# Optimization experiments

Hardware: AMD Instinct MI355X
Metric: run time of the kernel (lower is better)

## Reference

```python
import jax, jax.numpy as jnp
import numpy as np

B, T, E = 4096, 200, 64
H1, H2 = 80, 40


def setup_inputs() -> dict:
    key = jax.random.key(0)
    ks = jax.random.split(key, 9)
    query = jax.random.normal(ks[0], (B, 1, E), dtype=jnp.float32)
    keys = jax.random.normal(ks[1], (B, T, E), dtype=jnp.float32)
    keys_length = jax.random.randint(ks[2], (B,), 0, T, dtype=jnp.int64)
    # DNN params (init_std=1 in original, but any values work for a reference)
    W1 = jax.random.normal(ks[3], (4 * E, H1), dtype=jnp.float32) * 0.05
    b1 = jnp.zeros((H1,), dtype=jnp.float32)
    W2 = jax.random.normal(ks[4], (H1, H2), dtype=jnp.float32) * 0.05
    b2 = jnp.zeros((H2,), dtype=jnp.float32)
    Wd = jax.random.normal(ks[5], (H2, 1), dtype=jnp.float32) * 0.05
    bd = jnp.zeros((1,), dtype=jnp.float32)
    return {"query": query, "keys": keys, "keys_length": keys_length,
            "W1": W1, "b1": b1, "W2": W2, "b2": b2, "Wd": Wd, "bd": bd}


def reference(query, keys, keys_length, W1, b1, W2, b2, Wd, bd):
    # Local activation unit: expand query over T, build 4-way concat feature
    q = jnp.broadcast_to(query, keys.shape)                 # [B,T,E]
    att_in = jnp.concatenate([q, keys, q - keys, q * keys], axis=-1)  # [B,T,4E]
    # Small MLP with sigmoid activations (DNN), then linear head -> score
    h = jax.nn.sigmoid(jnp.einsum('btk,kh->bth', att_in, W1) + b1)
    h = jax.nn.sigmoid(jnp.einsum('btk,kh->bth', h, W2) + b2)
    score = jnp.einsum('btk,ko->bto', h, Wd) + bd           # [B,T,1]
    outputs = jnp.swapaxes(score, 1, 2)                     # [B,1,T]
    # length mask (supports_masking=False path)
    mask = (jnp.arange(keys.shape[1]) < keys_length[:, None])[:, None, :]  # [B,1,T]
    # weight_normalization=False -> masked positions get 0
    outputs = jnp.where(mask, outputs, jnp.zeros_like(outputs))
    # weighted sum pooling over history
    return jnp.matmul(outputs, keys)                        # [B,1,E]
```

## Files before the change

kernel.cpp:

```cpp
#include <hip/hip_runtime.h>

typedef float f32x4 __attribute__((ext_vector_type(4)));
typedef short bf16x8 __attribute__((ext_vector_type(8)));

#define T_LEN 200
#define E_DIM 64
#define H1D 80
#define H2D 40
#define T_PAD 208
#define NT1 5
#define NT2 3
#define WS_BC    0u
#define WS_D     20480u
#define WS_W2    40960u
#define WS_W1EFF 50176u
#define WS_BIAS  70656u

static __device__ __forceinline__ unsigned short f2bf(float x) {
  unsigned u = __builtin_bit_cast(unsigned, x);
  return (unsigned short)((u + 0x7fffu + ((u >> 16) & 1u)) >> 16);
}
static __device__ __forceinline__ float bf2f(unsigned short h) {
  unsigned u = ((unsigned)h) << 16;
  return __builtin_bit_cast(float, u);
}
static __device__ __forceinline__ float sigm(float x) {
  return __builtin_amdgcn_rcpf(1.f + __expf(-x));
}

__global__ __launch_bounds__(256)
void setup1(const float* __restrict__ W1, const float* __restrict__ W2,
            unsigned char* __restrict__ ws) {
  float* bc = (float*)(ws + WS_BC);
  float* dd = (float*)(ws + WS_D);
  unsigned short* w2f = (unsigned short*)(ws + WS_W2);
  float* w1e = (float*)(ws + WS_W1EFF);
  int g = blockIdx.x * 256 + threadIdx.x;
  if (g < 5120) {
    int nt = g >> 10;
    int rem = g & 1023;
    int ks = rem >> 9;
    int l = (rem >> 3) & 63;
    int j = g & 7;
    int e = ks * 32 + ((l >> 4) << 3) + j;
    int col = nt * 16 + (l & 15);
    bc[g] = W1[(64 + e) * H1D + col] - W1[(128 + e) * H1D + col];
    dd[g] = W1[(192 + e) * H1D + col];
  } else if (g < 9728) {
    int h = g - 5120;
    int nt2 = h / 1536;
    int rem = h - nt2 * 1536;
    int ks2 = rem >> 9;
    int l = (rem >> 3) & 63;
    int j = h & 7;
    int k = ks2 * 32 + ((l >> 4) << 3) + j;
    int n = nt2 * 16 + (l & 15);
    float v = (k < H1D && n < H2D) ? W2[k * H2D + n] : 0.f;
    w2f[h] = f2bf(v);
  } else if (g < 14848) {
    int w = g - 9728;
    int e = w / 80;
    int j = w - e * 80;
    w1e[w] = W1[e * H1D + j] + W1[(128 + e) * H1D + j];
  }
}

__global__ __launch_bounds__(128)
void setup2(const float* __restrict__ query, const float* __restrict__ b1,
            const unsigned char* __restrict__ ws, float* __restrict__ bias) {
  const float* w1e = (const float*)(ws + WS_W1EFF);
  const int b = blockIdx.x, j = threadIdx.x;
  if (j < H1D) {
    float s = b1[j];
    const float* q = query + (size_t)b * E_DIM;
    #pragma unroll
    for (int e = 0; e < E_DIM; ++e) s += q[e] * w1e[e * H1D + j];
    bias[(size_t)b * H1D + j] = s;
  }
}

#define OFF_K   0
#define OFF_H1  26624
#define OFF_FR  47104
#define OFF_SC  57344
#define OFF_PP  58176
#define OFF_QS  60224
#define OFF_B1  60480
#define SMEM_TOTAL 60800

template <bool BW>
__global__ __launch_bounds__(512, 2)
void din_main(const float* __restrict__ query, const float* __restrict__ keys,
              const int* __restrict__ keys_length,
              const float* __restrict__ b1, const float* __restrict__ b2,
              const float* __restrict__ Wd, const float* __restrict__ bd,
              const unsigned char* __restrict__ ws, float* __restrict__ out) {
  __shared__ __align__(16) unsigned char smem[SMEM_TOTAL];
  unsigned char* Kb  = smem + OFF_K;
  unsigned char* H1b = smem + OFF_H1;
  unsigned short* FR = (unsigned short*)(smem + OFF_FR);
  float* SC = (float*)(smem + OFF_SC);
  float* PP = (float*)(smem + OFF_PP);
  float* QS = (float*)(smem + OFF_QS);
  float* B1 = (float*)(smem + OFF_B1);

  const int tid = threadIdx.x, b = blockIdx.x;
  const int lane = tid & 63, wv = tid >> 6;
  const int qq = lane >> 4, cc = lane & 15;
  const float* keyb = keys + (size_t)b * (T_LEN * E_DIM);

  if (!BW && tid < E_DIM) QS[tid] = query[(size_t)b * E_DIM + tid];

  #pragma unroll
  for (int it = 0; it < 7; ++it) {
    int f = (it * 512 + tid) * 4;
    if (f < T_LEN * E_DIM) {
      const float4 v = *(const float4*)(keyb + f);
      unsigned p0 = ((unsigned)f2bf(v.y) << 16) | f2bf(v.x);
      unsigned p1 = ((unsigned)f2bf(v.w) << 16) | f2bf(v.z);
      int row = f >> 6;
      unsigned byte = ((unsigned)(f * 2)) ^ ((unsigned)(row & 7) << 4);
      *(uint2*)(Kb + byte) = make_uint2(p0, p1);
    } else if (f < T_PAD * E_DIM) {
      int row = f >> 6;
      unsigned byte = ((unsigned)(f * 2)) ^ ((unsigned)(row & 7) << 4);
      *(uint2*)(Kb + byte) = make_uint2(0u, 0u);
    }
  }

  {
    const float* wsBC = (const float*)(ws + WS_BC);
    const float* wsD  = (const float*)(ws + WS_D);
    const float* qrow = query + (size_t)b * E_DIM;
    #pragma unroll
    for (int i = 0; i < 10; ++i) {
      int f = i * 512 + tid;
      int j = f & 7, l = (f >> 3) & 63, ks = (f >> 9) & 1;
      int e = ks * 32 + ((l >> 4) << 3) + j;
      FR[f] = f2bf(wsBC[f] + qrow[e] * wsD[f]);
    }
  }

  float bia[NT1];
  if (BW) {
    const float* wbias = (const float*)(ws + WS_BIAS);
    #pragma unroll
    for (int nt = 0; nt < NT1; ++nt) bia[nt] = wbias[(size_t)b * H1D + nt * 16 + cc];
  }
  float b2c[NT2], wdl[NT2];
  #pragma unroll
  for (int nt = 0; nt < NT2; ++nt) {
    int col = nt * 16 + cc;
    b2c[nt] = (col < H2D) ? b2[col] : 0.f;
    wdl[nt] = (col < H2D) ? Wd[col] : 0.f;
  }
  const float bdv = bd[0];
  const int len = keys_length[b];

  __syncthreads();

  if (!BW) {
    if (tid < H1D) {
      const float* w1e = (const float*)(ws + WS_W1EFF);
      float s = b1[tid];
      #pragma unroll
      for (int e = 0; e < E_DIM; ++e) s += QS[e] * w1e[e * H1D + tid];
      B1[tid] = s;
    }
    __syncthreads();
    #pragma unroll
    for (int nt = 0; nt < NT1; ++nt) bia[nt] = B1[nt * 16 + cc];
  }

  const unsigned short* wsW2 = (const unsigned short*)(ws + WS_W2);
  unsigned char* H1w = H1b + wv * 2560;
  #pragma unroll
  for (int ti = 0; ti < 2; ++ti) {
    const int tt = wv + ti * 8;
    if (tt < 13) {
      const unsigned krow = (unsigned)(tt * 16 + cc);
      const unsigned ksw = (krow & 7u) << 4;
      bf16x8 a0 = *(const bf16x8*)(Kb + ((krow * 128 + qq * 16) ^ ksw));
      bf16x8 a1 = *(const bf16x8*)(Kb + ((krow * 128 + 64 + qq * 16) ^ ksw));
      f32x4 accs[NT1];
      #pragma unroll
      for (int nt = 0; nt < NT1; ++nt) {
        bf16x8 bf0 = *(const bf16x8*)(FR + ((nt * 2 + 0) * 64 + lane) * 8);
        bf16x8 bf1 = *(const bf16x8*)(FR + ((nt * 2 + 1) * 64 + lane) * 8);
        f32x4 a = {bia[nt], bia[nt], bia[nt], bia[nt]};
        a = __builtin_amdgcn_mfma_f32_16x16x32_bf16(a0, bf0, a, 0, 0, 0);
        a = __builtin_amdgcn_mfma_f32_16x16x32_bf16(a1, bf1, a, 0, 0, 0);
        accs[nt] = a;
      }
      #pragma unroll
      for (int nt = 0; nt < NT1; ++nt) {
        #pragma unroll
        for (int r = 0; r < 4; ++r) {
          int rloc = qq * 4 + r;
          unsigned byte = ((unsigned)(rloc * 160 + (nt * 16 + cc) * 2)) ^ ((unsigned)(rloc & 7) << 4);
          *(unsigned short*)(H1w + byte) = f2bf(sigm(accs[nt][r]));
        }
      }
      const unsigned hsw = ((unsigned)cc & 7u) << 4;
      const unsigned hb = (unsigned)cc * 160;
      bf16x8 h0 = *(const bf16x8*)(H1w + ((hb + qq * 16) ^ hsw));
      bf16x8 h1 = *(const bf16x8*)(H1w + ((hb + 64 + qq * 16) ^ hsw));
      bf16x8 h2 = {0, 0, 0, 0, 0, 0, 0, 0};
      if (qq < 2) h2 = *(const bf16x8*)(H1w + ((hb + 128 + qq * 16) ^ hsw));
      float vr[4] = {0.f, 0.f, 0.f, 0.f};
      #pragma unroll
      for (int nt = 0; nt < NT2; ++nt) {
        bf16x8 w0 = *(const bf16x8*)(wsW2 + ((nt * 3 + 0) * 64 + lane) * 8);
        bf16x8 w1 = *(const bf16x8*)(wsW2 + ((nt * 3 + 1) * 64 + lane) * 8);
        bf16x8 w2 = *(const bf16x8*)(wsW2 + ((nt * 3 + 2) * 64 + lane) * 8);
        f32x4 a = {b2c[nt], b2c[nt], b2c[nt], b2c[nt]};
        a = __builtin_amdgcn_mfma_f32_16x16x32_bf16(h0, w0, a, 0, 0, 0);
        a = __builtin_amdgcn_mfma_f32_16x16x32_bf16(h1, w1, a, 0, 0, 0);
        a = __builtin_amdgcn_mfma_f32_16x16x32_bf16(h2, w2, a, 0, 0, 0);
        #pragma unroll
        for (int r = 0; r < 4; ++r) vr[r] += sigm(a[r]) * wdl[nt];
      }
      #pragma unroll
      for (int r = 0; r < 4; ++r) {
        float v = vr[r];
        v += __shfl_xor(v, 1);
        v += __shfl_xor(v, 2);
        v += __shfl_xor(v, 4);
        v += __shfl_xor(v, 8);
        if (cc == 0) {
          int t = tt * 16 + qq * 4 + r;
          SC[t] = (t < len) ? (bdv + v) : 0.f;
        }
      }
    }
  }
  __syncthreads();

  {
    const int e = tid & 63;
    const int t0 = tid >> 6;
    float accp = 0.f;
    #pragma unroll
    for (int i = 0; i < 25; ++i) {
      int t = t0 + i * 8;
      float s = SC[t];
      unsigned byte = ((unsigned)(t * 128 + e * 2)) ^ ((unsigned)(t & 7) << 4);
      accp += s * bf2f(*(const unsigned short*)(Kb + byte));
    }
    PP[tid] = accp;
  }
  __syncthreads();
  if (tid < E_DIM) {
    float s = 0.f;
    #pragma unroll
    for (int w = 0; w < 8; ++w) s += PP[w * 64 + tid];
    out[(size_t)b * E_DIM + tid] = s;
  }
}

extern "C" void kernel_launch(void* const* d_in, const int* in_sizes, int n_in,
                              void* d_out, int out_size, void* d_ws, size_t ws_size,
                              hipStream_t stream) {
  const float* query = (const float*)d_in[0];
  const float* keys  = (const float*)d_in[1];
  const int*   klen  = (const int*)d_in[2];
  const float* W1 = (const float*)d_in[3];
  const float* b1 = (const float*)d_in[4];
  const float* W2 = (const float*)d_in[5];
  const float* b2 = (const float*)d_in[6];
  const float* Wd = (const float*)d_in[7];
  const float* bd = (const float*)d_in[8];
  float* out = (float*)d_out;
  const int B = in_sizes[2];
  unsigned char* ws = (unsigned char*)d_ws;

  hipLaunchKernelGGL(setup1, dim3(58), dim3(256), 0, stream, W1, W2, ws);

  const size_t needBias = (size_t)WS_BIAS + (size_t)B * H1D * 4;
  if (ws_size >= needBias) {
    hipLaunchKernelGGL(setup2, dim3(B), dim3(128), 0, stream,
                       query, b1, ws, (float*)(ws + WS_BIAS));
    din_main<true><<<dim3(B), dim3(512), 0, stream>>>(query, keys, klen, b1, b2, Wd, bd, ws, out);
  } else {
    din_main<false><<<dim3(B), dim3(512), 0, stream>>>(query, keys, klen, b1, b2, Wd, bd, ws, out);
  }
}
```

Baseline: 341.0 us.

## Load key MFMA fragments directly to registers and drop LDS key staging

Keys are no longer staged as bf16 in shared memory. Each wave loads its own MFMA A-fragments straight from global memory into registers, and the final weighted pooling re-reads the fp32 keys from global memory. The separate per-batch bias kernel (setup2) is removed and the bias is computed inside the main kernel, which cuts one launch and shrinks LDS use, possibly allowing more resident blocks. The cost is that keys are read from global memory twice (the second read likely hitting cache) and register pressure rises from holding the fragments.

```diff
diff --git a/kernel.cpp b/kernel.cpp
--- a/kernel.cpp
+++ b/kernel.cpp
@@ -2,27 +2,25 @@
 
 typedef float f32x4 __attribute__((ext_vector_type(4)));
 typedef short bf16x8 __attribute__((ext_vector_type(8)));
+typedef unsigned int uint;
 
 #define T_LEN 200
 #define E_DIM 64
 #define H1D 80
 #define H2D 40
-#define T_PAD 208
 #define NT1 5
 #define NT2 3
 #define WS_BC    0u
 #define WS_D     20480u
 #define WS_W2    40960u
 #define WS_W1EFF 50176u
-#define WS_BIAS  70656u
 
 static __device__ __forceinline__ unsigned short f2bf(float x) {
   unsigned u = __builtin_bit_cast(unsigned, x);
   return (unsigned short)((u + 0x7fffu + ((u >> 16) & 1u)) >> 16);
 }
-static __device__ __forceinline__ float bf2f(unsigned short h) {
-  unsigned u = ((unsigned)h) << 16;
-  return __builtin_bit_cast(float, u);
+static __device__ __forceinline__ uint pkbf(float lo, float hi) {
+  return ((uint)f2bf(hi) << 16) | (uint)f2bf(lo);
 }
 static __device__ __forceinline__ float sigm(float x) {
   return __builtin_amdgcn_rcpf(1.f + __expf(-x));
@@ -65,30 +63,12 @@
   }
 }
 
-__global__ __launch_bounds__(128)
-void setup2(const float* __restrict__ query, const float* __restrict__ b1,
-            const unsigned char* __restrict__ ws, float* __restrict__ bias) {
-  const float* w1e = (const float*)(ws + WS_W1EFF);
-  const int b = blockIdx.x, j = threadIdx.x;
-  if (j < H1D) {
-    float s = b1[j];
-    const float* q = query + (size_t)b * E_DIM;
-    #pragma unroll
-    for (int e = 0; e < E_DIM; ++e) s += q[e] * w1e[e * H1D + j];
-    bias[(size_t)b * H1D + j] = s;
-  }
-}
-
-#define OFF_K   0
-#define OFF_H1  26624
-#define OFF_FR  47104
-#define OFF_SC  57344
-#define OFF_PP  58176
-#define OFF_QS  60224
-#define OFF_B1  60480
-#define SMEM_TOTAL 60800
-
-template <bool BW>
+#define OFF_H1 0
+#define OFF_FR 20480
+#define OFF_SC 30720
+#define OFF_B1 31552
+#define SMEM_TOTAL 31872
+
 __global__ __launch_bounds__(512, 2)
 void din_main(const float* __restrict__ query, const float* __restrict__ keys,
               const int* __restrict__ keys_length,
@@ -96,57 +76,61 @@
               const float* __restrict__ Wd, const float* __restrict__ bd,
               const unsigned char* __restrict__ ws, float* __restrict__ out) {
   __shared__ __align__(16) unsigned char smem[SMEM_TOTAL];
-  unsigned char* Kb  = smem + OFF_K;
-  unsigned char* H1b = smem + OFF_H1;
   unsigned short* FR = (unsigned short*)(smem + OFF_FR);
   float* SC = (float*)(smem + OFF_SC);
-  float* PP = (float*)(smem + OFF_PP);
-  float* QS = (float*)(smem + OFF_QS);
   float* B1 = (float*)(smem + OFF_B1);
+  float* PP = (float*)(smem + OFF_FR);
 
   const int tid = threadIdx.x, b = blockIdx.x;
   const int lane = tid & 63, wv = tid >> 6;
   const int qq = lane >> 4, cc = lane & 15;
   const float* keyb = keys + (size_t)b * (T_LEN * E_DIM);
-
-  if (!BW && tid < E_DIM) QS[tid] = query[(size_t)b * E_DIM + tid];
-
+  const float* qrow = query + (size_t)b * E_DIM;
+
+  bf16x8 afr[2][2];
   #pragma unroll
-  for (int it = 0; it < 7; ++it) {
-    int f = (it * 512 + tid) * 4;
-    if (f < T_LEN * E_DIM) {
-      const float4 v = *(const float4*)(keyb + f);
-      unsigned p0 = ((unsigned)f2bf(v.y) << 16) | f2bf(v.x);
-      unsigned p1 = ((unsigned)f2bf(v.w) << 16) | f2bf(v.z);
-      int row = f >> 6;
-      unsigned byte = ((unsigned)(f * 2)) ^ ((unsigned)(row & 7) << 4);
-      *(uint2*)(Kb + byte) = make_uint2(p0, p1);
-    } else if (f < T_PAD * E_DIM) {
-      int row = f >> 6;
-      unsigned byte = ((unsigned)(f * 2)) ^ ((unsigned)(row & 7) << 4);
-      *(uint2*)(Kb + byte) = make_uint2(0u, 0u);
+  for (int ti = 0; ti < 2; ++ti) {
+    const int tt = wv + ti * 8;
+    const int row = tt * 16 + cc;
+    #pragma unroll
+    for (int ks = 0; ks < 2; ++ks) {
+      if (tt < 13 && row < T_LEN) {
+        const float4 va = *(const float4*)(keyb + row * E_DIM + ks * 32 + qq * 8);
+        const float4 vb = *(const float4*)(keyb + row * E_DIM + ks * 32 + qq * 8 + 4);
+        uint4 u;
+        u.x = pkbf(va.x, va.y);
+        u.y = pkbf(va.z, va.w);
+        u.z = pkbf(vb.x, vb.y);
+        u.w = pkbf(vb.z, vb.w);
+        afr[ti][ks] = __builtin_bit_cast(bf16x8, u);
+      } else {
+        afr[ti][ks] = bf16x8{0, 0, 0, 0, 0, 0, 0, 0};
+      }
     }
   }
 
   {
     const float* wsBC = (const float*)(ws + WS_BC);
     const float* wsD  = (const float*)(ws + WS_D);
-    const float* qrow = query + (size_t)b * E_DIM;
-    #pragma unroll
-    for (int i = 0; i < 10; ++i) {
-      int f = i * 512 + tid;
+    #pragma unroll
+    for (int i = 0; i < 5; ++i) {
+      int f = (i * 512 + tid) * 2;
       int j = f & 7, l = (f >> 3) & 63, ks = (f >> 9) & 1;
       int e = ks * 32 + ((l >> 4) << 3) + j;
-      FR[f] = f2bf(wsBC[f] + qrow[e] * wsD[f]);
-    }
-  }
-
-  float bia[NT1];
-  if (BW) {
-    const float* wbias = (const float*)(ws + WS_BIAS);
-    #pragma unroll
-    for (int nt = 0; nt < NT1; ++nt) bia[nt] = wbias[(size_t)b * H1D + nt * 16 + cc];
-  }
+      const float2 bc = *(const float2*)(wsBC + f);
+      const float2 dd = *(const float2*)(wsD + f);
+      *(uint*)(FR + f) = pkbf(bc.x + qrow[e] * dd.x, bc.y + qrow[e + 1] * dd.y);
+    }
+  }
+
+  if (tid < H1D) {
+    const float* w1e = (const float*)(ws + WS_W1EFF);
+    float s = b1[tid];
+    #pragma unroll
+    for (int e = 0; e < E_DIM; ++e) s += qrow[e] * w1e[e * H1D + tid];
+    B1[tid] = s;
+  }
+
   float b2c[NT2], wdl[NT2];
   #pragma unroll
   for (int nt = 0; nt < NT2; ++nt) {
@@ -159,46 +143,37 @@
 
   __syncthreads();
 
-  if (!BW) {
-    if (tid < H1D) {
-      const float* w1e = (const float*)(ws + WS_W1EFF);
-      float s = b1[tid];
-      #pragma unroll
-      for (int e = 0; e < E_DIM; ++e) s += QS[e] * w1e[e * H1D + tid];
-      B1[tid] = s;
-    }
-    __syncthreads();
-    #pragma unroll
-    for (int nt = 0; nt < NT1; ++nt) bia[nt] = B1[nt * 16 + cc];
-  }
+  float bia[NT1];
+  #pragma unroll
+  for (int nt = 0; nt < NT1; ++nt) bia[nt] = B1[nt * 16 + cc];
 
   const unsigned short* wsW2 = (const unsigned short*)(ws + WS_W2);
-  unsigned char* H1w = H1b + wv * 2560;
-  #pragma unroll
+  unsigned char* H1w = smem + OFF_H1 + wv * 2560;
+
+  #pragma unroll 1
   for (int ti = 0; ti < 2; ++ti) {
     const int tt = wv + ti * 8;
     if (tt < 13) {
-      const unsigned krow = (unsigned)(tt * 16 + cc);
-      const unsigned ksw = (krow & 7u) << 4;
-      bf16x8 a0 = *(const bf16x8*)(Kb + ((krow * 128 + qq * 16) ^ ksw));
-      bf16x8 a1 = *(const bf16x8*)(Kb + ((krow * 128 + 64 + qq * 16) ^ ksw));
       f32x4 accs[NT1];
       #pragma unroll
       for (int nt = 0; nt < NT1; ++nt) {
         bf16x8 bf0 = *(const bf16x8*)(FR + ((nt * 2 + 0) * 64 + lane) * 8);
         bf16x8 bf1 = *(const bf16x8*)(FR + ((nt * 2 + 1) * 64 + lane) * 8);
         f32x4 a = {bia[nt], bia[nt], bia[nt], bia[nt]};
-        a = __builtin_amdgcn_mfma_f32_16x16x32_bf16(a0, bf0, a, 0, 0, 0);
-        a = __builtin_amdgcn_mfma_f32_16x16x32_bf16(a1, bf1, a, 0, 0, 0);
+        a = __builtin_amdgcn_mfma_f32_16x16x32_bf16(afr[ti][0], bf0, a, 0, 0, 0);
+        a = __builtin_amdgcn_mfma_f32_16x16x32_bf16(afr[ti][1], bf1, a, 0, 0, 0);
         accs[nt] = a;
       }
       #pragma unroll
       for (int nt = 0; nt < NT1; ++nt) {
         #pragma unroll
-        for (int r = 0; r < 4; ++r) {
-          int rloc = qq * 4 + r;
-          unsigned byte = ((unsigned)(rloc * 160 + (nt * 16 + cc) * 2)) ^ ((unsigned)(rloc & 7) << 4);
-          *(unsigned short*)(H1w + byte) = f2bf(sigm(accs[nt][r]));
+        for (int r = 0; r < 4; r += 2) {
+          uint pk = pkbf(sigm(accs[nt][r]), sigm(accs[nt][r + 1]));
+          int r0 = qq * 4 + r, r1 = r0 + 1;
+          unsigned by0 = ((unsigned)(r0 * 160 + (nt * 16 + cc) * 2)) ^ ((unsigned)(r0 & 7) << 4);
+          unsigned by1 = ((unsigned)(r1 * 160 + (nt * 16 + cc) * 2)) ^ ((unsigned)(r1 & 7) << 4);
+          *(unsigned short*)(H1w + by0) = (unsigned short)pk;
+          *(unsigned short*)(H1w + by1) = (unsigned short)(pk >> 16);
         }
       }
       const unsigned hsw = ((unsigned)cc & 7u) << 4;
@@ -237,15 +212,12 @@
   __syncthreads();
 
   {
-    const int e = tid & 63;
-    const int t0 = tid >> 6;
+    const int e = lane;
     float accp = 0.f;
     #pragma unroll
     for (int i = 0; i < 25; ++i) {
-      int t = t0 + i * 8;
-      float s = SC[t];
-      unsigned byte = ((unsigned)(t * 128 + e * 2)) ^ ((unsigned)(t & 7) << 4);
-      accp += s * bf2f(*(const unsigned short*)(Kb + byte));
+      int t = wv + i * 8;
+      accp += SC[t] * keyb[t * E_DIM + e];
     }
     PP[tid] = accp;
   }
@@ -275,13 +247,6 @@
   unsigned char* ws = (unsigned char*)d_ws;
 
   hipLaunchKernelGGL(setup1, dim3(58), dim3(256), 0, stream, W1, W2, ws);
-
-  const size_t needBias = (size_t)WS_BIAS + (size_t)B * H1D * 4;
-  if (ws_size >= needBias) {
-    hipLaunchKernelGGL(setup2, dim3(B), dim3(128), 0, stream,
-                       query, b1, ws, (float*)(ws + WS_BIAS));
-    din_main<true><<<dim3(B), dim3(512), 0, stream>>>(query, keys, klen, b1, b2, Wd, bd, ws, out);
-  } else {
-    din_main<false><<<dim3(B), dim3(512), 0, stream>>>(query, keys, klen, b1, b2, Wd, bd, ws, out);
-  }
-}
+  hipLaunchKernelGGL(din_main, dim3(B), dim3(512), 0, stream,
+                     query, keys, klen, b1, b2, Wd, bd, ws, out);
+}
```

New measurement: 367.6 us. 7.8% more time.
